# Kernel tuning notes

Measured on AMD Instinct MI355X. Metric: run time of the kernel, lower is better.

Reference implementation:

```python
import jax, jax.numpy as jnp
import numpy as np

NUM_HEADS = 8
HEAD_DIM = 64
AVG_K_LENGTH = 20
SCALE = 1.0 / (HEAD_DIM ** 0.5 * float(np.log(AVG_K_LENGTH)))  # 1/(sqrt(dim)*log(avg_k_length))


def setup_inputs() -> dict:
    key = jax.random.key(0)
    k1, k2, k3, k4 = jax.random.split(key, 4)
    B, HD, LQ, LK = 4, NUM_HEADS * HEAD_DIM, 2048, 2048
    q = jax.random.normal(k1, (B, HD, LQ), dtype=jnp.float32)
    k = jax.random.normal(k2, (B, HD, LK), dtype=jnp.float32)
    v = jax.random.normal(k3, (B, HD, LK), dtype=jnp.float32)
    k_length = jax.random.randint(k4, (B,), 512, LK + 1, dtype=jnp.int32)
    return {"q": q, "k": k, "v": v, "k_length": k_length}


def reference(q, k, v, k_length):
    b, hd, lq = q.shape
    lk = k.shape[-1]
    d = hd // NUM_HEADS
    # b (h d) l -> b h d l
    qh = q.reshape(b, NUM_HEADS, d, lq)
    kh = k.reshape(b, NUM_HEADS, d, lk)
    vh = v.reshape(b, NUM_HEADS, d, lk)
    # per-batch entropy-invariance scale: scale * log(k_length)
    s = SCALE * jnp.log(k_length.astype(jnp.float32))[:, None, None, None]  # (b,1,1,1)
    attn = jnp.einsum('bhdq,bhdk->bhqk', qh, kh)  # (b,h,lq,lk)
    attn = jax.nn.softmax(s * attn, axis=-1)
    out = jnp.einsum('bhqk,bhdk->bhdq', attn, vh)  # (b,h,d,lq)
    return out.reshape(b, hd, lq)
```

## Files before the change

### kernel.cpp

```cpp
#include <hip/hip_runtime.h>
#include <hip/hip_bf16.h>
#include <math.h>


typedef __attribute__((ext_vector_type(8))) short short8_t;
typedef __attribute__((ext_vector_type(4))) short short4_t;
typedef __attribute__((ext_vector_type(4))) float float4_t;
typedef __attribute__((ext_vector_type(16))) float float16_t;

#define SEQ   2048
#define NBH   32
#define NKT   32

__device__ __forceinline__ unsigned f2bf2u(float a, float b) {
#if __has_builtin(__builtin_amdgcn_cvt_pk_bf16_f32)
  typedef __bf16 bf16x2_t __attribute__((ext_vector_type(2)));
  union { bf16x2_t v; unsigned u; } cv;
  cv.v = __builtin_amdgcn_cvt_pk_bf16_f32(a, b);
  return cv.u;
#else
  union { float f; unsigned u; } x, y;
  x.f = a; y.f = b;
  unsigned ra = x.u + 0x7fffu + ((x.u >> 16) & 1u);
  unsigned rb = y.u + 0x7fffu + ((y.u >> 16) & 1u);
  return (ra >> 16) | (rb & 0xffff0000u);
#endif
}

__device__ __forceinline__ short f2bf1(float a) {
  return (short)(f2bf2u(a, a) & 0xffffu);
}

__device__ __forceinline__ float fast_exp2(float x) {
#if __has_builtin(__builtin_amdgcn_exp2f)
  return __builtin_amdgcn_exp2f(x);
#else
  return exp2f(x);
#endif
}

__device__ __forceinline__ void gld16(const void* g, void* l) {
  __builtin_amdgcn_global_load_lds(
      (const __attribute__((address_space(1))) void*)g,
      (__attribute__((address_space(3))) void*)l, 16, 0, 0);
}

__device__ __forceinline__ float4_t mfma32(short8_t a, short8_t b, float4_t c) {
  return __builtin_amdgcn_mfma_f32_16x16x32_bf16(a, b, c, 0, 0, 0);
}

__device__ __forceinline__ float16_t mfma3232(short8_t a, short8_t b, float16_t c) {
  return __builtin_amdgcn_mfma_f32_32x32x16_bf16(a, b, c, 0, 0, 0);
}

__device__ __forceinline__ void plswap(unsigned& a, unsigned& b, int hi) {
#if __has_builtin(__builtin_amdgcn_permlane32_swap)
  typedef __attribute__((ext_vector_type(2))) unsigned uint2_t;
  uint2_t r = __builtin_amdgcn_permlane32_swap(a, b, false, false);
  a = r[0]; b = r[1];
#else
  const unsigned sa = (unsigned)__shfl_xor((int)a, 32);
  const unsigned sb = (unsigned)__shfl_xor((int)b, 32);
  const unsigned an = hi ? sb : a;
  const unsigned bn = hi ? b : sa;
  a = an; b = bn;
#endif
}

#define PST 68
__global__ __launch_bounds__(256, 8)
void eia_prep_kernel(const float* __restrict__ kg, const float* __restrict__ vg,
                     unsigned short* __restrict__ Kt2, unsigned short* __restrict__ Vt2) {
  __shared__ __align__(16) short T[64 * PST];
  const int bh = blockIdx.x >> 5;
  const int kt = blockIdx.x & 31;
  const int t  = threadIdx.x;

  {
    const int dr = t >> 4;
    const int kq = (t & 15) * 4;
#pragma unroll
    for (int i = 0; i < 4; ++i) {
      const int d = i * 16 + dr;
      const float4_t f = *(const float4_t*)
          &kg[((size_t)bh * 64 + d) * SEQ + (size_t)(kt * 64 + kq)];
      T[(kq + 0) * PST + d] = f2bf1(f[0]);
      T[(kq + 1) * PST + d] = f2bf1(f[1]);
      T[(kq + 2) * PST + d] = f2bf1(f[2]);
      T[(kq + 3) * PST + d] = f2bf1(f[3]);
    }
  }
  __syncthreads();
  {
    unsigned short* outt = Kt2 + (size_t)(bh * 32 + kt) * 4096;
#pragma unroll
    for (int rep = 0; rep < 2; ++rep) {
      const int id2 = rep * 256 + t;
      const int lr = id2 & 63, ch = id2 >> 6;
      union { short8_t v; short4_t h[2]; } o;
      o.h[0] = *(const short4_t*)&T[lr * PST + ch * 8];
      o.h[1] = *(const short4_t*)&T[lr * PST + ch * 8 + 4];
      *(short8_t*)&outt[ch * 512 + lr * 8] = o.v;
    }
  }
  __syncthreads();

#pragma unroll
  for (int rep = 0; rep < 4; ++rep) {
    const int id2 = rep * 256 + t;
    const int d = id2 >> 4, l4 = (id2 & 15) * 4;
    const float4_t f = *(const float4_t*)
        &vg[((size_t)bh * 64 + d) * SEQ + (size_t)(kt * 64 + l4)];
    union { short4_t s; unsigned u[2]; } p;
    p.u[0] = f2bf2u(f[0], f[1]);
    p.u[1] = f2bf2u(f[2], f[3]);
    *(short4_t*)&T[d * PST + l4] = p.s;
  }
  __syncthreads();
  {
    unsigned short* outt = Vt2 + (size_t)(bh * 32 + kt) * 4096;
#pragma unroll
    for (int rep = 0; rep < 2; ++rep) {
      const int c = rep * 256 + t;
      const int kc = c >> 6, d = c & 63;
      union { short8_t v; short4_t h[2]; } o;
      o.h[0] = *(const short4_t*)&T[d * PST + kc * 8];
      o.h[1] = *(const short4_t*)&T[d * PST + kc * 8 + 4];
      *(short8_t*)&outt[c * 8] = o.v;
    }
  }
}

__global__ __launch_bounds__(128, 2)
void eia_attn_kernel(const float* __restrict__ qg,
                     const unsigned short* __restrict__ Kt2,
                     const unsigned short* __restrict__ Vt2,
                     const int* __restrict__ klen,
                     float* __restrict__ outg) {
  __shared__ __align__(16) short SM[12288];

  const int tid   = threadIdx.x;
  const int bh    = blockIdx.x & 31;
  const int qt    = blockIdx.x >> 5;
  const int q0    = qt * 64;
  const int qw    = tid >> 6;
  const int lane  = tid & 63;
  const int l31   = lane & 31;
  const int hi    = lane >> 5;

  const float c = (1.4426950408889634f / (8.0f * 2.9957322735539909f)) *
                  logf((float)klen[bh >> 3]);
  const size_t qb = (size_t)bh * 64 * SEQ;

#pragma unroll
  for (int rep = 0; rep < 8; ++rep) {
    const int id = rep * 128 + tid;
    const int d  = id >> 4;
    const int q4 = (id & 15) * 4;
    const float4_t f = *(const float4_t*)&qg[qb + (size_t)d * SEQ + (size_t)(q0 + q4)];
    SM[(q4 + 0) * 68 + d] = f2bf1(c * f[0]);
    SM[(q4 + 1) * 68 + d] = f2bf1(c * f[1]);
    SM[(q4 + 2) * 68 + d] = f2bf1(c * f[2]);
    SM[(q4 + 3) * 68 + d] = f2bf1(c * f[3]);
  }
  __syncthreads();

  short8_t qfrag[4];
#pragma unroll
  for (int s = 0; s < 4; ++s) {
    const short* qp = &SM[(qw * 32 + l31) * 68 + s * 16 + hi * 8];
    const short4_t lo = *(const short4_t*)qp;
    const short4_t hh = *(const short4_t*)(qp + 4);
    qfrag[s] = short8_t{lo[0], lo[1], lo[2], lo[3], hh[0], hh[1], hh[2], hh[3]};
  }
  __syncthreads();

  const char* ksrc = (const char*)Kt2 + (size_t)bh * NKT * 8192 + (4 * qw) * 1024 + lane * 16;
  short* const kdst = &SM[(4 * qw) * 512];

  const int lofs = hi * 512 + l31 * 8;
  const short* const kfp = &SM[lofs];

  const char* const vgl = (const char*)Vt2 + (size_t)bh * NKT * 8192 +
                          hi * 1024 + l31 * 16;

  const float16_t z16 = {0.f,0.f,0.f,0.f,0.f,0.f,0.f,0.f,
                         0.f,0.f,0.f,0.f,0.f,0.f,0.f,0.f};
  float16_t oacc0 = z16, oacc1 = z16;
  float ls = 0.f;

  short8_t vA[8], vB[8];

#pragma unroll
  for (int i = 0; i < 4; ++i) gld16(ksrc + i * 1024, kdst + i * 512);
#pragma unroll
  for (int i = 0; i < 4; ++i) gld16(ksrc + 8192 + i * 1024, kdst + 4096 + i * 512);
#pragma unroll
  for (int dt = 0; dt < 2; ++dt)
#pragma unroll
    for (int ks = 0; ks < 4; ++ks)
      vA[dt * 4 + ks] = *(const short8_t*)(vgl + dt * 512 + ks * 2048);

  int  sc = 0;
  int  sn = 2;
  size_t gsrc = 2 * 8192;

#define EIA_BODY(KT, VC, VN)                                                  \
  do {                                                                        \
    asm volatile("s_waitcnt vmcnt(0)" ::: "memory");                          \
    asm volatile("s_barrier" ::: "memory");                                   \
    if ((KT) < NKT - 2) {                                                     \
      const int so = sn * 4096;                                               \
      _Pragma("unroll")                                                       \
      for (int i = 0; i < 4; ++i)                                             \
        gld16(ksrc + gsrc + i * 1024, kdst + so + i * 512);                   \
      gsrc += 8192;                                                           \
      sn = (sn == 2) ? 0 : sn + 1;                                            \
    }                                                                         \
    if ((KT) < NKT - 1) {                                                     \
      const char* vp = vgl + (size_t)((KT) + 1) * 8192;                       \
      _Pragma("unroll")                                                       \
      for (int dt = 0; dt < 2; ++dt)                                          \
        _Pragma("unroll")                                                     \
        for (int ks = 0; ks < 4; ++ks)                                        \
          VN[dt * 4 + ks] = *(const short8_t*)(vp + dt * 512 + ks * 2048);    \
    }                                                                         \
    const int koff = sc * 4096;                                               \
    sc = (sc == 2) ? 0 : sc + 1;                                              \
    const short* const kb_ = kfp + koff;                                      \
                   \
    float16_t s0 = z16, s1 = z16;                                             \
    _Pragma("unroll")                                                         \
    for (int s = 0; s < 4; ++s)                                               \
      s0 = mfma3232(*(const short8_t*)(kb_ + s * 1024), qfrag[s], s0);        \
    _Pragma("unroll")                                                         \
    for (int s = 0; s < 4; ++s)                                               \
      s1 = mfma3232(*(const short8_t*)(kb_ + 256 + s * 1024), qfrag[s], s1);  \
               \
    union pfu { short8_t s8; unsigned u[4]; };                                \
    pfu pf[4];                                                                \
    _Pragma("unroll")                                                         \
    for (int kb = 0; kb < 2; ++kb) {                                          \
      float e[16];                                                            \
      _Pragma("unroll")                                                       \
      for (int r = 0; r < 16; ++r)                                            \
        e[r] = fast_exp2(kb == 0 ? s0[r] : s1[r]);                            \
      ls += (((e[0] + e[1]) + (e[2] + e[3])) +                                \
             ((e[4] + e[5]) + (e[6] + e[7]))) +                               \
            (((e[8] + e[9]) + (e[10] + e[11])) +                              \
             ((e[12] + e[13]) + (e[14] + e[15])));                            \
      _Pragma("unroll")                                                       \
      for (int ksl = 0; ksl < 2; ++ksl) {                                     \
        const int b = ksl * 8;                                                \
        unsigned a02 = f2bf2u(e[b + 0], e[b + 1]);                            \
        unsigned b02 = f2bf2u(e[b + 4], e[b + 5]);                            \
        unsigned a13 = f2bf2u(e[b + 2], e[b + 3]);                            \
        unsigned b13 = f2bf2u(e[b + 6], e[b + 7]);                            \
        plswap(a02, b02, hi);                                                 \
        plswap(a13, b13, hi);                                                 \
        pf[kb * 2 + ksl].u[0] = a02;                                          \
        pf[kb * 2 + ksl].u[1] = a13;                                          \
        pf[kb * 2 + ksl].u[2] = b02;                                          \
        pf[kb * 2 + ksl].u[3] = b13;                                          \
      }                                                                       \
    }                                                                         \
           \
    _Pragma("unroll")                                                         \
    for (int ks = 0; ks < 4; ++ks)                                            \
      oacc0 = mfma3232(VC[ks], pf[ks].s8, oacc0);                             \
    _Pragma("unroll")                                                         \
    for (int ks = 0; ks < 4; ++ks)                                            \
      oacc1 = mfma3232(VC[4 + ks], pf[ks].s8, oacc1);                         \
  } while (0)

  for (int kt = 0; kt < NKT; kt += 2) {
    EIA_BODY(kt,     vA, vB);
    EIA_BODY(kt + 1, vB, vA);
  }
#undef EIA_BODY

  const float lst = ls + __shfl_xor(ls, 32);
  const float inv = 1.0f / lst;
  const size_t ob = qb + (size_t)(q0 + qw * 32 + l31);
#pragma unroll
  for (int r = 0; r < 16; ++r) {
    const int drow = (r & 3) + 8 * (r >> 2) + 4 * hi;
    outg[ob + (size_t)(drow) * SEQ]      = oacc0[r] * inv;
    outg[ob + (size_t)(drow + 32) * SEQ] = oacc1[r] * inv;
  }
}

#define DPAD  72
#define PPAD  68
__global__ __launch_bounds__(256, 5)
void eia_attn_fb(const float* __restrict__ qg, const float* __restrict__ kg,
                 const float* __restrict__ vg, const int* __restrict__ klen,
                 float* __restrict__ outg) {
  __shared__ __align__(16) short QPs[64 * DPAD];
  __shared__ __align__(16) short Ksf[64 * DPAD];
  __shared__ __align__(16) short Vsf[64 * DPAD];

  const int tid  = threadIdx.x;
  const int bh   = blockIdx.x & 31;
  const int qt   = blockIdx.x >> 5;
  const int q0   = qt * 64;
  const int w    = tid >> 6;
  const int lane = tid & 63;
  const int quad = lane >> 4;
  const int l16  = lane & 15;

  const size_t base = (size_t)bh * 64 * SEQ;
  const float c = (1.4426950408889634f / (8.0f * 2.9957322735539909f)) *
                  logf((float)klen[bh >> 3]);

#pragma unroll
  for (int it = 0; it < 2; ++it) {
    const int e = it * 4 + w;
    float f[8];
#pragma unroll
    for (int j = 0; j < 8; ++j)
      f[j] = c * qg[base + (size_t)(e * 8 + j) * SEQ + (size_t)(q0 + lane)];
    union { short8_t s8; unsigned u[4]; } t;
#pragma unroll
    for (int j = 0; j < 4; ++j) t.u[j] = f2bf2u(f[2 * j], f[2 * j + 1]);
    *(short8_t*)&QPs[lane * DPAD + e * 8] = t.s8;
  }
  __syncthreads();

  short8_t qfrag[2];
#pragma unroll
  for (int s = 0; s < 2; ++s)
    qfrag[s] = *(const short8_t*)&QPs[(w * 16 + l16) * DPAD + s * 32 + quad * 8];

  float4_t oacc[4];
#pragma unroll
  for (int t = 0; t < 4; ++t) { oacc[t][0] = 0.f; oacc[t][1] = 0.f; oacc[t][2] = 0.f; oacc[t][3] = 0.f; }
  float lsumv[4] = {0.f, 0.f, 0.f, 0.f};
  const int pbase = w * (16 * DPAD);

  for (int kt = 0; kt < NKT; ++kt) {
    const int k0 = kt * 64;
#pragma unroll
    for (int it = 0; it < 2; ++it) {
      float f[8];
#pragma unroll
      for (int j = 0; j < 8; ++j)
        f[j] = kg[base + (size_t)((it * 4 + w) * 8 + j) * SEQ + (size_t)(k0 + lane)];
      union { short8_t s8; unsigned u[4]; } t;
#pragma unroll
      for (int j = 0; j < 4; ++j) t.u[j] = f2bf2u(f[2 * j], f[2 * j + 1]);
      *(short8_t*)&Ksf[lane * DPAD + (it * 4 + w) * 8] = t.s8;
    }
#pragma unroll
    for (int it = 0; it < 4; ++it) {
      const int d = it * 16 + (w << 2) + (lane >> 4);
      const float4_t vv = *(const float4_t*)&vg[base + (size_t)d * SEQ + (size_t)(k0 + ((lane & 15) << 2))];
      union { short4_t s4; unsigned u[2]; } t;
      t.u[0] = f2bf2u(vv[0], vv[1]);
      t.u[1] = f2bf2u(vv[2], vv[3]);
      *(short4_t*)&Vsf[d * DPAD + ((lane & 15) << 2)] = t.s4;
    }
    __syncthreads();

    float4_t sacc[4];
#pragma unroll
    for (int t = 0; t < 4; ++t) { sacc[t][0] = 0.f; sacc[t][1] = 0.f; sacc[t][2] = 0.f; sacc[t][3] = 0.f; }
#pragma unroll
    for (int t = 0; t < 4; ++t)
#pragma unroll
      for (int s = 0; s < 2; ++s) {
        const short8_t bf = *(const short8_t*)&Ksf[(t * 16 + l16) * DPAD + s * 32 + quad * 8];
        sacc[t] = mfma32(qfrag[s], bf, sacc[t]);
      }

#pragma unroll
    for (int r = 0; r < 4; ++r) {
      const float p0 = fast_exp2(sacc[0][r]);
      const float p1 = fast_exp2(sacc[1][r]);
      const float p2 = fast_exp2(sacc[2][r]);
      const float p3 = fast_exp2(sacc[3][r]);
      lsumv[r] += (p0 + p1) + (p2 + p3);
      const int prow = pbase + (quad * 4 + r) * PPAD + l16;
      QPs[prow +  0] = f2bf1(p0);
      QPs[prow + 16] = f2bf1(p1);
      QPs[prow + 32] = f2bf1(p2);
      QPs[prow + 48] = f2bf1(p3);
    }

#pragma unroll
    for (int s = 0; s < 2; ++s) {
      const short* pr = &QPs[pbase + l16 * PPAD + s * 32 + quad * 8];
      const short4_t plo = *(const short4_t*)pr;
      const short4_t phi = *(const short4_t*)(pr + 4);
      const short8_t pfv = {plo[0], plo[1], plo[2], plo[3], phi[0], phi[1], phi[2], phi[3]};
#pragma unroll
      for (int t = 0; t < 4; ++t) {
        const short8_t vf = *(const short8_t*)&Vsf[(t * 16 + l16) * DPAD + s * 32 + quad * 8];
        oacc[t] = mfma32(pfv, vf, oacc[t]);
      }
    }
    __syncthreads();
  }

  float inv[4];
#pragma unroll
  for (int r = 0; r < 4; ++r) {
    float v = lsumv[r];
    v += __shfl_xor(v, 1);
    v += __shfl_xor(v, 2);
    v += __shfl_xor(v, 4);
    v += __shfl_xor(v, 8);
    inv[r] = 1.0f / v;
  }
#pragma unroll
  for (int t = 0; t < 4; ++t)
#pragma unroll
    for (int r = 0; r < 4; ++r)
      outg[base + (size_t)(t * 16 + l16) * SEQ +
           (size_t)(q0 + w * 16 + quad * 4 + r)] = oacc[t][r] * inv[r];
}

extern "C" void kernel_launch(void* const* d_in, const int* in_sizes, int n_in,
                              void* d_out, int out_size, void* d_ws, size_t ws_size,
                              hipStream_t stream) {
  const float* q  = (const float*)d_in[0];
  const float* k  = (const float*)d_in[1];
  const float* v  = (const float*)d_in[2];
  const int*   kl = (const int*)d_in[3];
  float* out = (float*)d_out;

  const size_t TEN  = (size_t)NBH * SEQ * 64;
  const size_t need = 2 * TEN * sizeof(unsigned short);

  if (ws_size >= need) {
    unsigned short* Kt2 = (unsigned short*)d_ws;
    unsigned short* Vt2 = Kt2 + TEN;
    eia_prep_kernel<<<1024, 256, 0, stream>>>(k, v, Kt2, Vt2);
    eia_attn_kernel<<<1024, 128, 0, stream>>>(q, Kt2, Vt2, kl, out);
  } else {
    eia_attn_fb<<<1024, 256, 0, stream>>>(q, k, v, kl, out);
  }
}
```

Baseline: 145.8 us.

## Stage V through shared memory with 4-wave 128-query blocks and interleaved tile pairs

```diff
diff --git a/kernel.cpp b/kernel.cpp
--- a/kernel.cpp
+++ b/kernel.cpp
@@ -131,18 +131,18 @@
   }
 }
 
-__global__ __launch_bounds__(128, 2)
+__global__ __launch_bounds__(256, 2)
 void eia_attn_kernel(const float* __restrict__ qg,
                      const unsigned short* __restrict__ Kt2,
                      const unsigned short* __restrict__ Vt2,
                      const int* __restrict__ klen,
                      float* __restrict__ outg) {
-  __shared__ __align__(16) short SM[12288];
+  __shared__ __align__(16) short SM[32768];
 
   const int tid   = threadIdx.x;
   const int bh    = blockIdx.x & 31;
   const int qt    = blockIdx.x >> 5;
-  const int q0    = qt * 64;
+  const int q0    = qt * 128;
   const int qw    = tid >> 6;
   const int lane  = tid & 63;
   const int l31   = lane & 31;
@@ -154,9 +154,9 @@
 
 #pragma unroll
   for (int rep = 0; rep < 8; ++rep) {
-    const int id = rep * 128 + tid;
-    const int d  = id >> 4;
-    const int q4 = (id & 15) * 4;
+    const int id = rep * 256 + tid;
+    const int d  = id >> 5;
+    const int q4 = (id & 31) * 4;
     const float4_t f = *(const float4_t*)&qg[qb + (size_t)d * SEQ + (size_t)(q0 + q4)];
     SM[(q4 + 0) * 68 + d] = f2bf1(c * f[0]);
     SM[(q4 + 1) * 68 + d] = f2bf1(c * f[1]);
@@ -175,76 +175,40 @@
   }
   __syncthreads();
 
-  const char* ksrc = (const char*)Kt2 + (size_t)bh * NKT * 8192 + (4 * qw) * 1024 + lane * 16;
-  short* const kdst = &SM[(4 * qw) * 512];
+  const char* ksrc = (const char*)Kt2 + (size_t)bh * NKT * 8192 + (2 * qw) * 1024 + lane * 16;
+  const char* vsrc = (const char*)Vt2 + (size_t)bh * NKT * 8192 + (2 * qw) * 1024 + lane * 16;
+  short* const kdst = &SM[(2 * qw) * 512];
+  short* const vdst = &SM[16384 + (2 * qw) * 512];
 
   const int lofs = hi * 512 + l31 * 8;
   const short* const kfp = &SM[lofs];
-
-  const char* const vgl = (const char*)Vt2 + (size_t)bh * NKT * 8192 +
-                          hi * 1024 + l31 * 16;
+  const short* const vfp = &SM[16384 + lofs];
 
   const float16_t z16 = {0.f,0.f,0.f,0.f,0.f,0.f,0.f,0.f,
                          0.f,0.f,0.f,0.f,0.f,0.f,0.f,0.f};
   float16_t oacc0 = z16, oacc1 = z16;
   float ls = 0.f;
 
-  short8_t vA[8], vB[8];
-
-#pragma unroll
-  for (int i = 0; i < 4; ++i) gld16(ksrc + i * 1024, kdst + i * 512);
-#pragma unroll
-  for (int i = 0; i < 4; ++i) gld16(ksrc + 8192 + i * 1024, kdst + 4096 + i * 512);
-#pragma unroll
-  for (int dt = 0; dt < 2; ++dt)
-#pragma unroll
-    for (int ks = 0; ks < 4; ++ks)
-      vA[dt * 4 + ks] = *(const short8_t*)(vgl + dt * 512 + ks * 2048);
-
-  int  sc = 0;
-  int  sn = 2;
-  size_t gsrc = 2 * 8192;
-
-#define EIA_BODY(KT, VC, VN)                                                  \
+  union pfu { short8_t s8; unsigned u[4]; };
+
+#define EIA_QK(KB, S0, S1)                                                    \
   do {                                                                        \
-    asm volatile("s_waitcnt vmcnt(0)" ::: "memory");                          \
-    asm volatile("s_barrier" ::: "memory");                                   \
-    if ((KT) < NKT - 2) {                                                     \
-      const int so = sn * 4096;                                               \
-      _Pragma("unroll")                                                       \
-      for (int i = 0; i < 4; ++i)                                             \
-        gld16(ksrc + gsrc + i * 1024, kdst + so + i * 512);                   \
-      gsrc += 8192;                                                           \
-      sn = (sn == 2) ? 0 : sn + 1;                                            \
-    }                                                                         \
-    if ((KT) < NKT - 1) {                                                     \
-      const char* vp = vgl + (size_t)((KT) + 1) * 8192;                       \
-      _Pragma("unroll")                                                       \
-      for (int dt = 0; dt < 2; ++dt)                                          \
-        _Pragma("unroll")                                                     \
-        for (int ks = 0; ks < 4; ++ks)                                        \
-          VN[dt * 4 + ks] = *(const short8_t*)(vp + dt * 512 + ks * 2048);    \
-    }                                                                         \
-    const int koff = sc * 4096;                                               \
-    sc = (sc == 2) ? 0 : sc + 1;                                              \
-    const short* const kb_ = kfp + koff;                                      \
-                   \
-    float16_t s0 = z16, s1 = z16;                                             \
     _Pragma("unroll")                                                         \
     for (int s = 0; s < 4; ++s)                                               \
-      s0 = mfma3232(*(const short8_t*)(kb_ + s * 1024), qfrag[s], s0);        \
+      S0 = mfma3232(*(const short8_t*)((KB) + s * 1024), qfrag[s], S0);       \
     _Pragma("unroll")                                                         \
     for (int s = 0; s < 4; ++s)                                               \
-      s1 = mfma3232(*(const short8_t*)(kb_ + 256 + s * 1024), qfrag[s], s1);  \
-               \
-    union pfu { short8_t s8; unsigned u[4]; };                                \
-    pfu pf[4];                                                                \
+      S1 = mfma3232(*(const short8_t*)((KB) + 256 + s * 1024), qfrag[s], S1); \
+  } while (0)
+
+#define EIA_EXPRP(S0, S1, PF)                                                 \
+  do {                                                                        \
     _Pragma("unroll")                                                         \
     for (int kb = 0; kb < 2; ++kb) {                                          \
       float e[16];                                                            \
       _Pragma("unroll")                                                       \
       for (int r = 0; r < 16; ++r)                                            \
-        e[r] = fast_exp2(kb == 0 ? s0[r] : s1[r]);                            \
+        e[r] = fast_exp2(kb == 0 ? S0[r] : S1[r]);                            \
       ls += (((e[0] + e[1]) + (e[2] + e[3])) +                                \
              ((e[4] + e[5]) + (e[6] + e[7]))) +                               \
             (((e[8] + e[9]) + (e[10] + e[11])) +                              \
@@ -258,26 +222,70 @@
         unsigned b13 = f2bf2u(e[b + 6], e[b + 7]);                            \
         plswap(a02, b02, hi);                                                 \
         plswap(a13, b13, hi);                                                 \
-        pf[kb * 2 + ksl].u[0] = a02;                                          \
-        pf[kb * 2 + ksl].u[1] = a13;                                          \
-        pf[kb * 2 + ksl].u[2] = b02;                                          \
-        pf[kb * 2 + ksl].u[3] = b13;                                          \
+        PF[kb * 2 + ksl].u[0] = a02;                                          \
+        PF[kb * 2 + ksl].u[1] = a13;                                          \
+        PF[kb * 2 + ksl].u[2] = b02;                                          \
+        PF[kb * 2 + ksl].u[3] = b13;                                          \
       }                                                                       \
     }                                                                         \
-           \
+  } while (0)
+
+#define EIA_PV(VB, PF)                                                        \
+  do {                                                                        \
     _Pragma("unroll")                                                         \
     for (int ks = 0; ks < 4; ++ks)                                            \
-      oacc0 = mfma3232(VC[ks], pf[ks].s8, oacc0);                             \
+      oacc0 = mfma3232(*(const short8_t*)((VB) + ks * 1024), PF[ks].s8, oacc0);\
     _Pragma("unroll")                                                         \
     for (int ks = 0; ks < 4; ++ks)                                            \
-      oacc1 = mfma3232(VC[4 + ks], pf[ks].s8, oacc1);                         \
+      oacc1 = mfma3232(*(const short8_t*)((VB) + 256 + ks * 1024),            \
+                       PF[ks].s8, oacc1);                                     \
   } while (0)
 
-  for (int kt = 0; kt < NKT; kt += 2) {
-    EIA_BODY(kt,     vA, vB);
-    EIA_BODY(kt + 1, vB, vA);
-  }
-#undef EIA_BODY
+#pragma unroll
+  for (int i = 0; i < 2; ++i) {
+    const size_t gb = (size_t)i * 8192;
+    const int so = i * 4096;
+    gld16(ksrc + gb, kdst + so); gld16(ksrc + gb + 1024, kdst + so + 512);
+    gld16(vsrc + gb, vdst + so); gld16(vsrc + gb + 1024, vdst + so + 512);
+  }
+
+  int sc = 0;
+  size_t gsrc = 16384;
+
+  for (int p = 0; p < NKT / 2; ++p) {
+    asm volatile("s_waitcnt vmcnt(0)" ::: "memory");
+    asm volatile("s_barrier" ::: "memory");
+
+    if (p < NKT / 2 - 1) {
+      const int so = (sc ^ 1) * 8192;
+#pragma unroll
+      for (int i = 0; i < 2; ++i) {
+        gld16(ksrc + gsrc + (size_t)i * 8192, kdst + so + i * 4096);
+        gld16(ksrc + gsrc + (size_t)i * 8192 + 1024, kdst + so + i * 4096 + 512);
+        gld16(vsrc + gsrc + (size_t)i * 8192, vdst + so + i * 4096);
+        gld16(vsrc + gsrc + (size_t)i * 8192 + 1024, vdst + so + i * 4096 + 512);
+      }
+      gsrc += 16384;
+    }
+    const int koff = sc * 8192;
+    sc ^= 1;
+    const short* const kb0 = kfp + koff;
+    const short* const vb0 = vfp + koff;
+    const short* const kb1 = kb0 + 4096;
+    const short* const vb1 = vb0 + 4096;
+
+    float16_t s0a = z16, s1a = z16, s0b = z16, s1b = z16;
+    pfu pf0[4], pf1[4];
+    EIA_QK(kb0, s0a, s1a);
+    EIA_EXPRP(s0a, s1a, pf0);
+    EIA_QK(kb1, s0b, s1b);
+    EIA_PV(vb0, pf0);
+    EIA_EXPRP(s0b, s1b, pf1);
+    EIA_PV(vb1, pf1);
+  }
+#undef EIA_QK
+#undef EIA_EXPRP
+#undef EIA_PV
 
   const float lst = ls + __shfl_xor(ls, 32);
   const float inv = 1.0f / lst;
@@ -436,7 +444,7 @@
     unsigned short* Kt2 = (unsigned short*)d_ws;
     unsigned short* Vt2 = Kt2 + TEN;
     eia_prep_kernel<<<1024, 256, 0, stream>>>(k, v, Kt2, Vt2);
-    eia_attn_kernel<<<1024, 128, 0, stream>>>(q, Kt2, Vt2, kl, out);
+    eia_attn_kernel<<<512, 256, 0, stream>>>(q, Kt2, Vt2, kl, out);
   } else {
     eia_attn_fb<<<1024, 256, 0, stream>>>(q, k, v, kl, out);
   }
```

Result: faster. 140.1 us (-3.9%).
